# Optimization experiments

Measured on AMD Instinct MI355X. Metric: run time of the kernel, lower is better.

## Reference

```python
import jax, jax.numpy as jnp
import numpy as np

B, N, D = 256, 16384, 7
NUM_CLASSES = 3
EPS = 1e-6


def setup_inputs() -> dict:
    key = jax.random.key(0)
    k1, k2, k3, k4 = jax.random.split(key, 4)
    # predictions: objectness prob, x, y, size all in (0,1); class logits also rand
    output = jax.random.uniform(k1, (B, N, D), dtype=jnp.float32, minval=0.01, maxval=0.99)
    obj = (jax.random.uniform(k2, (B, N)) < 0.5).astype(jnp.float32)
    coords = jax.random.uniform(k3, (B, N, 3), dtype=jnp.float32, minval=0.01, maxval=0.99)
    cls = jax.random.randint(k4, (B, N), 0, NUM_CLASSES).astype(jnp.float32)
    pad = jnp.zeros((B, N, 2), dtype=jnp.float32)
    target = jnp.concatenate([obj[..., None], coords, cls[..., None], pad], axis=-1)
    return {"output": output, "target": target}


def _iou_square(px, py, ps, tx, ty, ts):
    # boxes are (center_x, center_y, side); w == h == side
    lx = jnp.maximum(px - ps / 2, tx - ts / 2)
    rx = jnp.minimum(px + ps / 2, tx + ts / 2)
    ly = jnp.maximum(py - ps / 2, ty - ts / 2)
    ry = jnp.minimum(py + ps / 2, ty + ts / 2)
    inter = jnp.clip(rx - lx, 0.0) * jnp.clip(ry - ly, 0.0)
    union = ps * ps + ts * ts - inter
    return inter / (union + EPS)


def reference(output, target):
    p_obj = output[..., 0]
    px, py, ps = output[..., 1], output[..., 2], output[..., 3]
    t_obj = target[..., 0]
    tx, ty, ts = target[..., 1], target[..., 2], target[..., 3]
    m = (t_obj > 0.5).astype(output.dtype)  # object mask

    box = (tx - px) ** 2 + (ty - py) ** 2 + 2.0 * (jnp.sqrt(ts) - jnp.sqrt(ps)) ** 2

    # objectness BCE against IoU target
    iou = _iou_square(px, py, ps, tx, ty, ts)
    bce_obj = -(iou * jnp.log(p_obj) + (1.0 - iou) * jnp.log(1.0 - p_obj))

    # class CE against one-hot target (soft-target CE == log_softmax gather)
    logp = jax.nn.log_softmax(output[..., 4:7], axis=-1)
    t_cls = target[..., 4].astype(jnp.int32)
    ce = -jnp.take_along_axis(logp, t_cls[..., None], axis=-1)[..., 0]

    # no-object BCE against target objectness (0 where mask is off)
    bce_noobj = -(t_obj * jnp.log(p_obj) + (1.0 - t_obj) * jnp.log(1.0 - p_obj))

    boxLoss = jnp.sum(box * m)
    objectLoss = jnp.sum(bce_obj * m)
    classLoss = jnp.sum(ce * m)
    noObjectLoss = jnp.sum(bce_noobj * (1.0 - m))
    return 5.0 * boxLoss + 2.0 * classLoss + objectLoss + 1.5 * noObjectLoss
```

## Files before the change

kernel.cpp:

```cpp
#include <hip/hip_runtime.h>
#include <hip/hip_bf16.h>


#define RB 256
#define RN 16384
#define RD 7
#define NREC (RB * RN)
#define BLOCK 256
#define GRID 2048

__global__ __launch_bounds__(BLOCK) void loss_partial_kernel(
    const float* __restrict__ out, const float* __restrict__ tgt,
    float* __restrict__ partial) {
    __shared__ float so[BLOCK * RD];
    __shared__ float st[BLOCK * RD];

    float acc = 0.0f;
    const int t = threadIdx.x;

    for (int base = blockIdx.x * BLOCK; base < NREC; base += GRID * BLOCK) {
        const int gbase = base * RD;
        __syncthreads();
#pragma unroll
        for (int k = 0; k < RD; ++k) {
            so[k * BLOCK + t] = out[gbase + k * BLOCK + t];
            st[k * BLOCK + t] = tgt[gbase + k * BLOCK + t];
        }
        __syncthreads();

        const float* ro = &so[t * RD];
        const float* rt = &st[t * RD];

        const float p_obj = ro[0];
        const float px = ro[1], py = ro[2], ps = ro[3];
        const float l0 = ro[4], l1 = ro[5], l2 = ro[6];
        const float t_obj = rt[0];
        const float tx = rt[1], ty = rt[2], ts = rt[3];
        const float cls = rt[4];

        const float m = (t_obj > 0.5f) ? 1.0f : 0.0f;

        const float dx = tx - px, dy = ty - py;
        const float dsz = __fsqrt_rn(ts) - __fsqrt_rn(ps);
        const float box = dx * dx + dy * dy + 2.0f * dsz * dsz;

        const float hp = 0.5f * ps, ht = 0.5f * ts;
        const float lx = fmaxf(px - hp, tx - ht);
        const float rx = fminf(px + hp, tx + ht);
        const float ly = fmaxf(py - hp, ty - ht);
        const float ry = fminf(py + hp, ty + ht);
        const float inter = fmaxf(rx - lx, 0.0f) * fmaxf(ry - ly, 0.0f);
        const float uni = ps * ps + ts * ts - inter;
        const float iou = inter / (uni + 1e-6f);

        const float logp  = __logf(p_obj);
        const float log1p = __logf(1.0f - p_obj);

        const float bce_obj = -(iou * logp + (1.0f - iou) * log1p);

        const float mx = fmaxf(fmaxf(l0, l1), l2);
        const float esum = __expf(l0 - mx) + __expf(l1 - mx) + __expf(l2 - mx);
        const float lse = mx + __logf(esum);
        const float lcls = (cls < 0.5f) ? l0 : ((cls < 1.5f) ? l1 : l2);
        const float ce = lse - lcls;

        const float bce_noobj = -(t_obj * logp + (1.0f - t_obj) * log1p);

        acc += m * (5.0f * box + 2.0f * ce + bce_obj)
             + 1.5f * (1.0f - m) * bce_noobj;
    }

#pragma unroll
    for (int off = 32; off > 0; off >>= 1) acc += __shfl_down(acc, off);

    __shared__ float wsum[BLOCK / 64];
    if ((t & 63) == 0) wsum[t >> 6] = acc;
    __syncthreads();
    if (t == 0) {
        float s = 0.0f;
#pragma unroll
        for (int w = 0; w < BLOCK / 64; ++w) s += wsum[w];
        partial[blockIdx.x] = s;
    }
}

__global__ __launch_bounds__(BLOCK) void reduce_final_kernel(
    const float* __restrict__ partial, float* __restrict__ outp, int n) {
    float a = 0.0f;
    for (int i = threadIdx.x; i < n; i += BLOCK) a += partial[i];
#pragma unroll
    for (int off = 32; off > 0; off >>= 1) a += __shfl_down(a, off);
    __shared__ float wsum[BLOCK / 64];
    if ((threadIdx.x & 63) == 0) wsum[threadIdx.x >> 6] = a;
    __syncthreads();
    if (threadIdx.x == 0) {
        float s = 0.0f;
#pragma unroll
        for (int w = 0; w < BLOCK / 64; ++w) s += wsum[w];
        outp[0] = s;
    }
}

extern "C" void kernel_launch(void* const* d_in, const int* in_sizes, int n_in,
                              void* d_out, int out_size, void* d_ws, size_t ws_size,
                              hipStream_t stream) {
    const float* out = (const float*)d_in[0];
    const float* tgt = (const float*)d_in[1];
    float* partial = (float*)d_ws;
    float* result = (float*)d_out;

    loss_partial_kernel<<<GRID, BLOCK, 0, stream>>>(out, tgt, partial);
    reduce_final_kernel<<<1, BLOCK, 0, stream>>>(partial, result, GRID);
}
```

Baseline: 42.32 us.

## Vectorize loads, prefetch next tile, fuse final reduction via last-block atomic

The staging loads become float4 global loads with fully unrolled iterations. The next tile is prefetched into registers while the current tile is computed, so memory latency overlaps with math. The separate reduction kernel is removed: each block publishes its partial sum, and the last block to increment an atomic counter reduces all partials. In exchange, a memset of the counter is added to each launch, and the last block's reduction runs serially at the tail.

```diff
diff --git a/kernel.cpp b/kernel.cpp
--- a/kernel.cpp
+++ b/kernel.cpp
@@ -2,30 +2,47 @@
 #include <hip/hip_bf16.h>
 
 
-#define RB 256
-#define RN 16384
 #define RD 7
-#define NREC (RB * RN)
+#define NRECTOT (256 * 16384)
 #define BLOCK 256
 #define GRID 2048
+#define ITERS (NRECTOT / (GRID * BLOCK))
+#define STEP (GRID * BLOCK)
+#define F4T ((BLOCK * RD) / 4)
 
-__global__ __launch_bounds__(BLOCK) void loss_partial_kernel(
+__global__ __launch_bounds__(BLOCK) void loss_kernel(
     const float* __restrict__ out, const float* __restrict__ tgt,
-    float* __restrict__ partial) {
-    __shared__ float so[BLOCK * RD];
-    __shared__ float st[BLOCK * RD];
+    float* __restrict__ partial, unsigned int* __restrict__ counter,
+    float* __restrict__ result) {
+    __shared__ float4 so4[F4T];
+    __shared__ float4 st4[F4T];
+    const float* so = (const float*)so4;
+    const float* st = (const float*)st4;
+    const float4* og = (const float4*)out;
+    const float4* tg = (const float4*)tgt;
+
+    const int t = threadIdx.x;
+    const bool second = (t < F4T - BLOCK);
 
     float acc = 0.0f;
-    const int t = threadIdx.x;
+    int base = blockIdx.x * BLOCK;
 
-    for (int base = blockIdx.x * BLOCK; base < NREC; base += GRID * BLOCK) {
-        const int gbase = base * RD;
+    int g4 = (base * RD) >> 2;
+    float4 ro0 = og[g4 + t], rt0 = tg[g4 + t];
+    float4 ro1{}, rt1{};
+    if (second) { ro1 = og[g4 + BLOCK + t]; rt1 = tg[g4 + BLOCK + t]; }
+
+#pragma unroll
+    for (int i = 0; i < ITERS; ++i) {
+        float4 no0{}, nt0{}, no1{}, nt1{};
+        if (i + 1 < ITERS) {
+            const int ng4 = ((base + STEP) * RD) >> 2;
+            no0 = og[ng4 + t]; nt0 = tg[ng4 + t];
+            if (second) { no1 = og[ng4 + BLOCK + t]; nt1 = tg[ng4 + BLOCK + t]; }
+        }
         __syncthreads();
-#pragma unroll
-        for (int k = 0; k < RD; ++k) {
-            so[k * BLOCK + t] = out[gbase + k * BLOCK + t];
-            st[k * BLOCK + t] = tgt[gbase + k * BLOCK + t];
-        }
+        so4[t] = ro0; st4[t] = rt0;
+        if (second) { so4[BLOCK + t] = ro1; st4[BLOCK + t] = rt1; }
         __syncthreads();
 
         const float* ro = &so[t * RD];
@@ -68,36 +85,37 @@
 
         acc += m * (5.0f * box + 2.0f * ce + bce_obj)
              + 1.5f * (1.0f - m) * bce_noobj;
+
+        ro0 = no0; rt0 = nt0; ro1 = no1; rt1 = nt1;
+        base += STEP;
     }
 
 #pragma unroll
     for (int off = 32; off > 0; off >>= 1) acc += __shfl_down(acc, off);
-
     __shared__ float wsum[BLOCK / 64];
+    __shared__ bool amLast;
     if ((t & 63) == 0) wsum[t >> 6] = acc;
     __syncthreads();
     if (t == 0) {
-        float s = 0.0f;
+        float s = wsum[0] + wsum[1] + wsum[2] + wsum[3];
+        __hip_atomic_store(&partial[blockIdx.x], s, __ATOMIC_RELAXED,
+                           __HIP_MEMORY_SCOPE_AGENT);
+        unsigned int old = __hip_atomic_fetch_add(counter, 1u, __ATOMIC_ACQ_REL,
+                                                  __HIP_MEMORY_SCOPE_AGENT);
+        amLast = (old == GRID - 1);
+    }
+    __syncthreads();
+    if (amLast) {
+        float a = 0.0f;
 #pragma unroll
-        for (int w = 0; w < BLOCK / 64; ++w) s += wsum[w];
-        partial[blockIdx.x] = s;
-    }
-}
-
-__global__ __launch_bounds__(BLOCK) void reduce_final_kernel(
-    const float* __restrict__ partial, float* __restrict__ outp, int n) {
-    float a = 0.0f;
-    for (int i = threadIdx.x; i < n; i += BLOCK) a += partial[i];
+        for (int k = 0; k < GRID / BLOCK; ++k)
+            a += __hip_atomic_load(&partial[k * BLOCK + t], __ATOMIC_RELAXED,
+                                   __HIP_MEMORY_SCOPE_AGENT);
 #pragma unroll
-    for (int off = 32; off > 0; off >>= 1) a += __shfl_down(a, off);
-    __shared__ float wsum[BLOCK / 64];
-    if ((threadIdx.x & 63) == 0) wsum[threadIdx.x >> 6] = a;
-    __syncthreads();
-    if (threadIdx.x == 0) {
-        float s = 0.0f;
-#pragma unroll
-        for (int w = 0; w < BLOCK / 64; ++w) s += wsum[w];
-        outp[0] = s;
+        for (int off = 32; off > 0; off >>= 1) a += __shfl_down(a, off);
+        if ((t & 63) == 0) wsum[t >> 6] = a;
+        __syncthreads();
+        if (t == 0) result[0] = wsum[0] + wsum[1] + wsum[2] + wsum[3];
     }
 }
 
@@ -106,9 +124,12 @@
                               hipStream_t stream) {
     const float* out = (const float*)d_in[0];
     const float* tgt = (const float*)d_in[1];
-    float* partial = (float*)d_ws;
     float* result = (float*)d_out;
 
-    loss_partial_kernel<<<GRID, BLOCK, 0, stream>>>(out, tgt, partial);
-    reduce_final_kernel<<<1, BLOCK, 0, stream>>>(partial, result, GRID);
+    unsigned int* counter = (unsigned int*)d_ws;
+    float* partial = (float*)((char*)d_ws + 256);
+
+    hipMemsetAsync(counter, 0, sizeof(unsigned int), stream);
+
+    loss_kernel<<<GRID, BLOCK, 0, stream>>>(out, tgt, partial, counter, result);
 }
```

Result: slower. 81.26 us (+92.0%).

## Load four records per thread with float4 vector loads, dropping LDS staging

Applied to the files above, without the earlier changes.

Each thread now reads four whole records (28 floats) straight from global memory using seven float4 loads per input into registers, replacing the grid-stride loop that staged data through shared memory behind two barriers per iteration. The grid grows to one thread per four records, so there are many more blocks and no loop. This is meant to remove the shared-memory round trip and the barriers and to issue wider loads. In exchange, per-thread float4 accesses are strided by 112 bytes across lanes, so coalescing is weaker, and the extra registers may lower occupancy.

```diff
diff --git a/kernel.cpp b/kernel.cpp
--- a/kernel.cpp
+++ b/kernel.cpp
@@ -2,73 +2,73 @@
 #include <hip/hip_bf16.h>
 
 
-#define RB 256
-#define RN 16384
 #define RD 7
-#define NREC (RB * RN)
+#define NRECTOT (256 * 16384)
 #define BLOCK 256
-#define GRID 2048
+#define RPT 4
+#define NTHREADS (NRECTOT / RPT)
+#define GRID (NTHREADS / BLOCK)
+
+__device__ __forceinline__ float record_loss(const float* ro, const float* rt) {
+    const float p_obj = ro[0];
+    const float px = ro[1], py = ro[2], ps = ro[3];
+    const float l0 = ro[4], l1 = ro[5], l2 = ro[6];
+    const float t_obj = rt[0];
+    const float tx = rt[1], ty = rt[2], ts = rt[3];
+    const float cls = rt[4];
+
+    const float m = (t_obj > 0.5f) ? 1.0f : 0.0f;
+
+    const float dx = tx - px, dy = ty - py;
+    const float dsz = __fsqrt_rn(ts) - __fsqrt_rn(ps);
+    const float box = dx * dx + dy * dy + 2.0f * dsz * dsz;
+
+    const float hp = 0.5f * ps, ht = 0.5f * ts;
+    const float lx = fmaxf(px - hp, tx - ht);
+    const float rx = fminf(px + hp, tx + ht);
+    const float ly = fmaxf(py - hp, ty - ht);
+    const float ry = fminf(py + hp, ty + ht);
+    const float inter = fmaxf(rx - lx, 0.0f) * fmaxf(ry - ly, 0.0f);
+    const float uni = ps * ps + ts * ts - inter;
+    const float iou = inter / (uni + 1e-6f);
+
+    const float logp  = __logf(p_obj);
+    const float log1p = __logf(1.0f - p_obj);
+
+    const float bce_obj = -(iou * logp + (1.0f - iou) * log1p);
+
+    const float mx = fmaxf(fmaxf(l0, l1), l2);
+    const float esum = __expf(l0 - mx) + __expf(l1 - mx) + __expf(l2 - mx);
+    const float lse = mx + __logf(esum);
+    const float lcls = (cls < 0.5f) ? l0 : ((cls < 1.5f) ? l1 : l2);
+    const float ce = lse - lcls;
+
+    const float bce_noobj = -(t_obj * logp + (1.0f - t_obj) * log1p);
+
+    return m * (5.0f * box + 2.0f * ce + bce_obj)
+         + 1.5f * (1.0f - m) * bce_noobj;
+}
 
 __global__ __launch_bounds__(BLOCK) void loss_partial_kernel(
     const float* __restrict__ out, const float* __restrict__ tgt,
     float* __restrict__ partial) {
-    __shared__ float so[BLOCK * RD];
-    __shared__ float st[BLOCK * RD];
+    const int t = threadIdx.x;
+    const int tid = blockIdx.x * BLOCK + t;
+
+    const float4* og = (const float4*)out + (size_t)tid * RD;
+    const float4* tg = (const float4*)tgt + (size_t)tid * RD;
+
+    float vo[RPT * RD], vt[RPT * RD];
+#pragma unroll
+    for (int k = 0; k < RD; ++k) {
+        *(float4*)&vo[4 * k] = og[k];
+        *(float4*)&vt[4 * k] = tg[k];
+    }
 
     float acc = 0.0f;
-    const int t = threadIdx.x;
-
-    for (int base = blockIdx.x * BLOCK; base < NREC; base += GRID * BLOCK) {
-        const int gbase = base * RD;
-        __syncthreads();
 #pragma unroll
-        for (int k = 0; k < RD; ++k) {
-            so[k * BLOCK + t] = out[gbase + k * BLOCK + t];
-            st[k * BLOCK + t] = tgt[gbase + k * BLOCK + t];
-        }
-        __syncthreads();
-
-        const float* ro = &so[t * RD];
-        const float* rt = &st[t * RD];
-
-        const float p_obj = ro[0];
-        const float px = ro[1], py = ro[2], ps = ro[3];
-        const float l0 = ro[4], l1 = ro[5], l2 = ro[6];
-        const float t_obj = rt[0];
-        const float tx = rt[1], ty = rt[2], ts = rt[3];
-        const float cls = rt[4];
-
-        const float m = (t_obj > 0.5f) ? 1.0f : 0.0f;
-
-        const float dx = tx - px, dy = ty - py;
-        const float dsz = __fsqrt_rn(ts) - __fsqrt_rn(ps);
-        const float box = dx * dx + dy * dy + 2.0f * dsz * dsz;
-
-        const float hp = 0.5f * ps, ht = 0.5f * ts;
-        const float lx = fmaxf(px - hp, tx - ht);
-        const float rx = fminf(px + hp, tx + ht);
-        const float ly = fmaxf(py - hp, ty - ht);
-        const float ry = fminf(py + hp, ty + ht);
-        const float inter = fmaxf(rx - lx, 0.0f) * fmaxf(ry - ly, 0.0f);
-        const float uni = ps * ps + ts * ts - inter;
-        const float iou = inter / (uni + 1e-6f);
-
-        const float logp  = __logf(p_obj);
-        const float log1p = __logf(1.0f - p_obj);
-
-        const float bce_obj = -(iou * logp + (1.0f - iou) * log1p);
-
-        const float mx = fmaxf(fmaxf(l0, l1), l2);
-        const float esum = __expf(l0 - mx) + __expf(l1 - mx) + __expf(l2 - mx);
-        const float lse = mx + __logf(esum);
-        const float lcls = (cls < 0.5f) ? l0 : ((cls < 1.5f) ? l1 : l2);
-        const float ce = lse - lcls;
-
-        const float bce_noobj = -(t_obj * logp + (1.0f - t_obj) * log1p);
-
-        acc += m * (5.0f * box + 2.0f * ce + bce_obj)
-             + 1.5f * (1.0f - m) * bce_noobj;
-    }
+    for (int j = 0; j < RPT; ++j)
+        acc += record_loss(&vo[j * RD], &vt[j * RD]);
 
 #pragma unroll
     for (int off = 32; off > 0; off >>= 1) acc += __shfl_down(acc, off);
@@ -76,12 +76,8 @@
     __shared__ float wsum[BLOCK / 64];
     if ((t & 63) == 0) wsum[t >> 6] = acc;
     __syncthreads();
-    if (t == 0) {
-        float s = 0.0f;
-#pragma unroll
-        for (int w = 0; w < BLOCK / 64; ++w) s += wsum[w];
-        partial[blockIdx.x] = s;
-    }
+    if (t == 0)
+        partial[blockIdx.x] = wsum[0] + wsum[1] + wsum[2] + wsum[3];
 }
 
 __global__ __launch_bounds__(BLOCK) void reduce_final_kernel(
@@ -93,12 +89,8 @@
     __shared__ float wsum[BLOCK / 64];
     if ((threadIdx.x & 63) == 0) wsum[threadIdx.x >> 6] = a;
     __syncthreads();
-    if (threadIdx.x == 0) {
-        float s = 0.0f;
-#pragma unroll
-        for (int w = 0; w < BLOCK / 64; ++w) s += wsum[w];
-        outp[0] = s;
-    }
+    if (threadIdx.x == 0)
+        outp[0] = wsum[0] + wsum[1] + wsum[2] + wsum[3];
 }
 
 extern "C" void kernel_launch(void* const* d_in, const int* in_sizes, int n_in,
```

Measured after the change: 44.85 us. 6.0% more time.
